# Kernel tuning notes

Measured on AMD Instinct MI355X. Metric: run time of the kernel, lower is better.

Reference implementation:

```python
import jax, jax.numpy as jnp
import numpy as np

BN_EPS = 1e-5


def setup_inputs() -> dict:
    key = jax.random.key(0)
    ks = jax.random.split(key, 8)
    N, C, T, V, M = 32, 64, 300, 25, 2
    O, S = 64, 3  # out_channels, num_subset
    x = jax.random.normal(ks[0], (N, C, T, V, M), jnp.float32)
    PA = jax.random.normal(ks[1], (S, V, V), jnp.float32) * 0.1
    conv_w = jax.random.normal(ks[2], (O * S, C), jnp.float32) * (1.0 / np.sqrt(C))
    conv_b = jax.random.normal(ks[3], (O * S,), jnp.float32) * 0.01
    bn_gamma = jnp.ones((O,), jnp.float32)
    bn_beta = jnp.zeros((O,), jnp.float32)
    bn_mean = jax.random.normal(ks[4], (O,), jnp.float32) * 0.1
    bn_var = jax.random.uniform(ks[5], (O,), jnp.float32, 0.5, 1.5)
    return {"x": x, "PA": PA, "conv_w": conv_w, "conv_b": conv_b,
            "bn_gamma": bn_gamma, "bn_beta": bn_beta,
            "bn_mean": bn_mean, "bn_var": bn_var}


def reference(x, PA, conv_w, conv_b, bn_gamma, bn_beta, bn_mean, bn_var):
    N, C, T, V, M = x.shape
    S = PA.shape[0]
    O = conv_w.shape[0] // S
    # (N, C, T, V, M) -> (N*M, C, T, V)
    xb = jnp.transpose(x, (0, 4, 1, 2, 3)).reshape(N * M, C, T, V)
    res = xb  # identity residual (in_channels == out_channels, stride == 1)
    # 1x1 conv == per-position matmul over channels
    y = jnp.einsum('bctv,oc->botv', xb, conv_w) + conv_b[None, :, None, None]
    y = y.reshape(N * M, S, O, T, V)
    # sum over subsets of per-subset adjacency mixes (fused einsum)
    z = jnp.einsum('bsctv,svw->bctw', y, PA)
    # BatchNorm2d (inference form with running stats)
    scale = bn_gamma / jnp.sqrt(bn_var + BN_EPS)
    z = z * scale[None, :, None, None] + (bn_beta - bn_mean * scale)[None, :, None, None]
    z = jax.nn.relu(z)
    out = jax.nn.relu(z + res)
    # (N*M, O, T, V) -> (N, O, T, V, M)
    return jnp.transpose(out.reshape(N, M, O, T, V), (0, 2, 3, 4, 1))
```

## Files before the change

### kernel.cpp

```cpp
#include <hip/hip_runtime.h>
#include <cstddef>
#include <cstdint>

#define N_  32
#define C_  64
#define T_  300
#define V_  25
#define M_  2
#define S_  3
#define O_  64
#define OS_ 192
#define TB  6
#define NT_BLK (T_/TB)
#define CTVM (C_*T_*V_*M_)
#define TVM  (T_*V_*M_)
#define VM   (V_*M_)
#define XPITCH 72
#define YPITCH 72

typedef short  short8  __attribute__((ext_vector_type(8)));
typedef float  float4_ __attribute__((ext_vector_type(4)));

__device__ __forceinline__ short f2bf(float f) {
    uint32_t u = __float_as_uint(f);
    u += 0x7FFFu + ((u >> 16) & 1u);
    return (short)(u >> 16);
}
__device__ __forceinline__ unsigned pk2bf(float a, float b) {
    const uint32_t ua = (uint32_t)(uint16_t)f2bf(a);
    const uint32_t ub = (uint32_t)(uint16_t)f2bf(b);
    return ua | (ub << 16);
}

__global__ void stgcn_prep(const float* __restrict__ Wc, const float* __restrict__ PA,
                           const float* __restrict__ g,  const float* __restrict__ b,
                           const float* __restrict__ mn, const float* __restrict__ vr,
                           short* __restrict__ Wb, short* __restrict__ PAb,
                           float* __restrict__ scl, float* __restrict__ sft)
{
    const int i = blockIdx.x * 256 + threadIdx.x;
    if (i < OS_ * C_) Wb[i] = f2bf(Wc[i]);
    const int r = i - OS_ * C_;
    if (r >= 0 && r < S_ * 32 * 32) {
        const int s = r >> 10, rem = r & 1023, wp = rem >> 5, vp = rem & 31;
        const float val = (wp < V_ && vp < V_) ? PA[s * V_ * V_ + vp * V_ + wp] : 0.0f;
        PAb[r] = f2bf(val);
    }
    const int q = r - S_ * 32 * 32;
    if (q >= 0 && q < O_) {
        const float sc = g[q] * rsqrtf(vr[q] + 1e-5f);
        scl[q] = sc;
        sft[q] = b[q] - mn[q] * sc;
    }
}

__global__ __launch_bounds__(256, 3)
void stgcn_main(const float* __restrict__ x, const float* __restrict__ cb,
                const short* __restrict__ Wb, const short* __restrict__ PAb,
                const float* __restrict__ sclg, const float* __restrict__ sftg,
                float* __restrict__ out)
{
    __shared__ short Xb[2][64 * XPITCH];
    __shared__ short Ys[OS_ * YPITCH];
    __shared__ float sclS[O_], sftS[O_];

    const int tid  = threadIdx.x;
    const int wv   = tid >> 6;
    const int lane = tid & 63;
    const int quad = lane >> 4;
    const int l15  = lane & 15;

    const int n  = blockIdx.x / NT_BLK;
    const int t0 = (blockIdx.x % NT_BLK) * TB;
    const size_t xbase = (size_t)n * CTVM;

    for (int i = tid; i < 2 * 14 * XPITCH; i += 256) {
        const int bf = i / (14 * XPITCH);
        const int r  = i - bf * (14 * XPITCH);
        const int pr = r / XPITCH, cc = r - pr * XPITCH;
        const int pos = (pr < 7) ? (25 + pr) : (50 + pr);
        Xb[bf][pos * XPITCH + cc] = 0;
    }
    if (tid < O_) { sclS[tid] = sclg[tid]; sftS[tid] = sftg[tid]; }

    const int wbase = wv * 48;
    short8 aW[3][2];
    #pragma unroll
    for (int mt = 0; mt < 3; ++mt)
        #pragma unroll
        for (int ks = 0; ks < 2; ++ks)
            aW[mt][ks] = *(const short8*)(Wb + (wbase + mt * 16 + l15) * C_ + ks * 32 + quad * 8);

    const int m2 = wv >> 1, hh = wv & 1;
    short8 bP[3];
    #pragma unroll
    for (int s = 0; s < 3; ++s)
        bP[s] = *(const short8*)(PAb + (s * 1024 + (hh * 16 + l15) * 32 + quad * 8));

    float cbw[3];
    #pragma unroll
    for (int mt = 0; mt < 3; ++mt) cbw[mt] = cb[wbase + mt * 16 + l15];

    {
        const float* xt = x + xbase + (size_t)t0 * VM;
        #pragma unroll
        for (int k = 0; k < 4; ++k) {
            const int p = tid + k * 256;
            if (p < 800) {
                const int v = p % 25, cp = p / 25;
                const float2 f0 = *(const float2*)(xt + (size_t)(2 * cp)     * TVM + v * 2);
                const float2 f1 = *(const float2*)(xt + (size_t)(2 * cp + 1) * TVM + v * 2);
                ((unsigned*)Xb[0])[v * 36 + cp]        = pk2bf(f0.x, f1.x);
                ((unsigned*)Xb[0])[(32 + v) * 36 + cp] = pk2bf(f0.y, f1.y);
            }
        }
    }

    int cur = 0;
    for (int tt = 0; tt < TB; ++tt) {
        __syncthreads();

        float2 R0[4], R1[4];
        const bool pf = (tt + 1 < TB);
        if (pf) {
            const float* xt = x + xbase + (size_t)(t0 + tt + 1) * VM;
            #pragma unroll
            for (int k = 0; k < 4; ++k) {
                const int p = tid + k * 256;
                if (p < 800) {
                    const int v = p % 25, cp = p / 25;
                    R0[k] = *(const float2*)(xt + (size_t)(2 * cp)     * TVM + v * 2);
                    R1[k] = *(const float2*)(xt + (size_t)(2 * cp + 1) * TVM + v * 2);
                }
            }
        }

        const short* Xc = Xb[cur];
        short8 bX[4][2];
        #pragma unroll
        for (int nt = 0; nt < 4; ++nt)
            #pragma unroll
            for (int ks = 0; ks < 2; ++ks)
                bX[nt][ks] = *(const short8*)(Xc + (nt * 16 + l15) * XPITCH + ks * 32 + quad * 8);

        #pragma unroll
        for (int mt = 0; mt < 3; ++mt) {
            #pragma unroll
            for (int nt = 0; nt < 4; ++nt) {
                float4_ acc = { cbw[mt], cbw[mt], cbw[mt], cbw[mt] };
                acc = __builtin_amdgcn_mfma_f32_16x16x32_bf16(bX[nt][0], aW[mt][0], acc, 0, 0, 0);
                acc = __builtin_amdgcn_mfma_f32_16x16x32_bf16(bX[nt][1], aW[mt][1], acc, 0, 0, 0);
                const int os = wbase + mt * 16 + l15;
                *(uint2*)(Ys + os * YPITCH + nt * 16 + quad * 4) =
                    make_uint2(pk2bf(acc[0], acc[1]), pk2bf(acc[2], acc[3]));
            }
        }
        __syncthreads();

        float4_ z[4];
        #pragma unroll
        for (int ot = 0; ot < 4; ++ot) { z[ot][0]=0.f; z[ot][1]=0.f; z[ot][2]=0.f; z[ot][3]=0.f; }
        #pragma unroll
        for (int s = 0; s < 3; ++s) {
            #pragma unroll
            for (int ot = 0; ot < 4; ++ot) {
                const short8 aY = *(const short8*)(Ys + (s * 64 + ot * 16 + l15) * YPITCH + m2 * 32 + quad * 8);
                z[ot] = __builtin_amdgcn_mfma_f32_16x16x32_bf16(aY, bP[s], z[ot], 0, 0, 0);
            }
        }

        const int wc = hh * 16 + l15;
        const int t  = t0 + tt;
        if (wc < V_) {
            const int xrow = (m2 * 32 + wc) * XPITCH;
            #pragma unroll
            for (int ot = 0; ot < 4; ++ot) {
                #pragma unroll
                for (int r = 0; r < 4; ++r) {
                    const int o = ot * 16 + quad * 4 + r;
                    const float res = __uint_as_float(((unsigned)(unsigned short)Xc[xrow + o]) << 16);
                    float q = fmaf(z[ot][r], sclS[o], sftS[o]);
                    q = fmaxf(q, 0.0f);
                    q = fmaxf(q + res, 0.0f);
                    out[xbase + (size_t)o * TVM + (size_t)t * VM + wc * 2 + m2] = q;
                }
            }
        }

        if (pf) {
            short* Xn = Xb[cur ^ 1];
            #pragma unroll
            for (int k = 0; k < 4; ++k) {
                const int p = tid + k * 256;
                if (p < 800) {
                    const int v = p % 25, cp = p / 25;
                    ((unsigned*)Xn)[v * 36 + cp]        = pk2bf(R0[k].x, R1[k].x);
                    ((unsigned*)Xn)[(32 + v) * 36 + cp] = pk2bf(R0[k].y, R1[k].y);
                }
            }
        }
        cur ^= 1;
    }
}

extern "C" void kernel_launch(void* const* d_in, const int* in_sizes, int n_in,
                              void* d_out, int out_size, void* d_ws, size_t ws_size,
                              hipStream_t stream)
{
    const float* x    = (const float*)d_in[0];
    const float* PA   = (const float*)d_in[1];
    const float* Wc   = (const float*)d_in[2];
    const float* cb   = (const float*)d_in[3];
    const float* bn_g = (const float*)d_in[4];
    const float* bn_b = (const float*)d_in[5];
    const float* bn_m = (const float*)d_in[6];
    const float* bn_v = (const float*)d_in[7];
    float* out = (float*)d_out;

    char* ws = (char*)d_ws;
    short* Wb  = (short*)ws;
    short* PAb = (short*)(ws + 24576);
    float* scl = (float*)(ws + 30720);
    float* sft = (float*)(ws + 30976);

    stgcn_prep<<<61, 256, 0, stream>>>(Wc, PA, bn_g, bn_b, bn_m, bn_v, Wb, PAb, scl, sft);
    stgcn_main<<<N_ * NT_BLK, 256, 0, stream>>>(x, cb, Wb, PAb, scl, sft, out);
}
```

Measured before the change: 289.5 us.

## Fuse prep into main kernel, use per-wave Y staging, deepen x prefetch

Drops the separate prep launch: each block now converts the weights, adjacency matrix and BN parameters to bf16/scale form directly from fp32 inputs. The work is repartitioned so each wave computes all three subsets for its own 16 output channels and stages Y in a private LDS slice. This removes the mid-iteration block-wide barrier, leaving only one barrier per time step. Global x prefetch goes two timesteps ahead, and stores are paired across M into float2 writes. In exchange, every block repeats the parameter conversion and holds more registers for the prefetch buffers, which may pressure occupancy.

```diff
diff --git a/kernel.cpp b/kernel.cpp
--- a/kernel.cpp
+++ b/kernel.cpp
@@ -9,7 +9,6 @@
 #define M_  2
 #define S_  3
 #define O_  64
-#define OS_ 192
 #define TB  6
 #define NT_BLK (T_/TB)
 #define CTVM (C_*T_*V_*M_)
@@ -27,41 +26,24 @@
     return (short)(u >> 16);
 }
 __device__ __forceinline__ unsigned pk2bf(float a, float b) {
-    const uint32_t ua = (uint32_t)(uint16_t)f2bf(a);
-    const uint32_t ub = (uint32_t)(uint16_t)f2bf(b);
-    return ua | (ub << 16);
-}
-
-__global__ void stgcn_prep(const float* __restrict__ Wc, const float* __restrict__ PA,
-                           const float* __restrict__ g,  const float* __restrict__ b,
-                           const float* __restrict__ mn, const float* __restrict__ vr,
-                           short* __restrict__ Wb, short* __restrict__ PAb,
-                           float* __restrict__ scl, float* __restrict__ sft)
-{
-    const int i = blockIdx.x * 256 + threadIdx.x;
-    if (i < OS_ * C_) Wb[i] = f2bf(Wc[i]);
-    const int r = i - OS_ * C_;
-    if (r >= 0 && r < S_ * 32 * 32) {
-        const int s = r >> 10, rem = r & 1023, wp = rem >> 5, vp = rem & 31;
-        const float val = (wp < V_ && vp < V_) ? PA[s * V_ * V_ + vp * V_ + wp] : 0.0f;
-        PAb[r] = f2bf(val);
-    }
-    const int q = r - S_ * 32 * 32;
-    if (q >= 0 && q < O_) {
-        const float sc = g[q] * rsqrtf(vr[q] + 1e-5f);
-        scl[q] = sc;
-        sft[q] = b[q] - mn[q] * sc;
-    }
+    return (uint32_t)(uint16_t)f2bf(a) | ((uint32_t)(uint16_t)f2bf(b) << 16);
+}
+__device__ __forceinline__ void barrier_lgkm() {
+    asm volatile("s_waitcnt lgkmcnt(0)\n\ts_barrier" ::: "memory");
+}
+__device__ __forceinline__ void wait_lgkm() {
+    asm volatile("s_waitcnt lgkmcnt(0)" ::: "memory");
 }
 
 __global__ __launch_bounds__(256, 3)
-void stgcn_main(const float* __restrict__ x, const float* __restrict__ cb,
-                const short* __restrict__ Wb, const short* __restrict__ PAb,
-                const float* __restrict__ sclg, const float* __restrict__ sftg,
-                float* __restrict__ out)
+void stgcn_fused(const float* __restrict__ x,  const float* __restrict__ PA,
+                 const float* __restrict__ Wc, const float* __restrict__ cb,
+                 const float* __restrict__ g,  const float* __restrict__ bb,
+                 const float* __restrict__ mn, const float* __restrict__ vr,
+                 float* __restrict__ out)
 {
     __shared__ short Xb[2][64 * XPITCH];
-    __shared__ short Ys[OS_ * YPITCH];
+    __shared__ short Ysw[4 * 48 * YPITCH];
     __shared__ float sclS[O_], sftS[O_];
 
     const int tid  = threadIdx.x;
@@ -69,10 +51,70 @@
     const int lane = tid & 63;
     const int quad = lane >> 4;
     const int l15  = lane & 15;
+    const int ybase = wv * 48 * YPITCH;
 
     const int n  = blockIdx.x / NT_BLK;
     const int t0 = (blockIdx.x % NT_BLK) * TB;
     const size_t xbase = (size_t)n * CTVM;
+
+    float2 P0[4], P1[4];
+    float2 Rx[2][4], Ry[2][4];
+    {
+        const float* xt = x + xbase + (size_t)t0 * VM;
+        #pragma unroll
+        for (int k = 0; k < 4; ++k) {
+            const int p = tid + k * 256;
+            if (p < 800) {
+                const int v = p % 25, cp = p / 25;
+                P0[k] = *(const float2*)(xt + (size_t)(2 * cp)     * TVM + v * 2);
+                P1[k] = *(const float2*)(xt + (size_t)(2 * cp + 1) * TVM + v * 2);
+                Rx[0][k] = *(const float2*)(xt + (size_t)(2 * cp)     * TVM + VM + v * 2);
+                Ry[0][k] = *(const float2*)(xt + (size_t)(2 * cp + 1) * TVM + VM + v * 2);
+            }
+        }
+    }
+
+    short8 aW[3][2];
+    #pragma unroll
+    for (int s = 0; s < 3; ++s)
+        #pragma unroll
+        for (int ks = 0; ks < 2; ++ks) {
+            const float* wr = Wc + (size_t)(s * 64 + wv * 16 + l15) * C_ + ks * 32 + quad * 8;
+            const float4 wa = *(const float4*)wr;
+            const float4 wb = *(const float4*)(wr + 4);
+            union { short8 s8; unsigned u[4]; } r;
+            r.u[0] = pk2bf(wa.x, wa.y); r.u[1] = pk2bf(wa.z, wa.w);
+            r.u[2] = pk2bf(wb.x, wb.y); r.u[3] = pk2bf(wb.z, wb.w);
+            aW[s][ks] = r.s8;
+        }
+
+    short8 bP[3][2];
+    #pragma unroll
+    for (int s = 0; s < 3; ++s)
+        #pragma unroll
+        for (int wt = 0; wt < 2; ++wt) {
+            const int w = wt * 16 + l15;
+            float pv[8];
+            #pragma unroll
+            for (int j = 0; j < 8; ++j) {
+                const int v = quad * 8 + j;
+                pv[j] = (w < V_ && v < V_) ? PA[s * V_ * V_ + v * V_ + w] : 0.0f;
+            }
+            union { short8 s8; unsigned u[4]; } r;
+            r.u[0] = pk2bf(pv[0], pv[1]); r.u[1] = pk2bf(pv[2], pv[3]);
+            r.u[2] = pk2bf(pv[4], pv[5]); r.u[3] = pk2bf(pv[6], pv[7]);
+            bP[s][wt] = r.s8;
+        }
+
+    float cbw[3];
+    #pragma unroll
+    for (int s = 0; s < 3; ++s) cbw[s] = cb[s * 64 + wv * 16 + l15];
+
+    if (tid < O_) {
+        const float sc = g[tid] * rsqrtf(vr[tid] + 1e-5f);
+        sclS[tid] = sc;
+        sftS[tid] = bb[tid] - mn[tid] * sc;
+    }
 
     for (int i = tid; i < 2 * 14 * XPITCH; i += 256) {
         const int bf = i / (14 * XPITCH);
@@ -81,56 +123,37 @@
         const int pos = (pr < 7) ? (25 + pr) : (50 + pr);
         Xb[bf][pos * XPITCH + cc] = 0;
     }
-    if (tid < O_) { sclS[tid] = sclg[tid]; sftS[tid] = sftg[tid]; }
-
-    const int wbase = wv * 48;
-    short8 aW[3][2];
-    #pragma unroll
-    for (int mt = 0; mt < 3; ++mt)
-        #pragma unroll
-        for (int ks = 0; ks < 2; ++ks)
-            aW[mt][ks] = *(const short8*)(Wb + (wbase + mt * 16 + l15) * C_ + ks * 32 + quad * 8);
-
-    const int m2 = wv >> 1, hh = wv & 1;
-    short8 bP[3];
-    #pragma unroll
-    for (int s = 0; s < 3; ++s)
-        bP[s] = *(const short8*)(PAb + (s * 1024 + (hh * 16 + l15) * 32 + quad * 8));
-
-    float cbw[3];
-    #pragma unroll
-    for (int mt = 0; mt < 3; ++mt) cbw[mt] = cb[wbase + mt * 16 + l15];
-
-    {
-        const float* xt = x + xbase + (size_t)t0 * VM;
-        #pragma unroll
-        for (int k = 0; k < 4; ++k) {
-            const int p = tid + k * 256;
-            if (p < 800) {
-                const int v = p % 25, cp = p / 25;
-                const float2 f0 = *(const float2*)(xt + (size_t)(2 * cp)     * TVM + v * 2);
-                const float2 f1 = *(const float2*)(xt + (size_t)(2 * cp + 1) * TVM + v * 2);
-                ((unsigned*)Xb[0])[v * 36 + cp]        = pk2bf(f0.x, f1.x);
-                ((unsigned*)Xb[0])[(32 + v) * 36 + cp] = pk2bf(f0.y, f1.y);
-            }
-        }
-    }
-
-    int cur = 0;
-    for (int tt = 0; tt < TB; ++tt) {
-        __syncthreads();
-
-        float2 R0[4], R1[4];
-        const bool pf = (tt + 1 < TB);
-        if (pf) {
-            const float* xt = x + xbase + (size_t)(t0 + tt + 1) * VM;
+
+    #pragma unroll
+    for (int k = 0; k < 4; ++k) {
+        const int p = tid + k * 256;
+        if (p < 800) {
+            const int v = p % 25, cp = p / 25;
+            ((unsigned*)Xb[0])[v * 36 + cp]        = pk2bf(P0[k].x, P1[k].x);
+            ((unsigned*)Xb[0])[(32 + v) * 36 + cp] = pk2bf(P0[k].y, P1[k].y);
+        }
+    }
+    barrier_lgkm();
+
+    const float4 sclr = *(const float4*)&sclS[wv * 16 + quad * 4];
+    const float4 sftr = *(const float4*)&sftS[wv * 16 + quad * 4];
+    const float sclA[4] = { sclr.x, sclr.y, sclr.z, sclr.w };
+    const float sftA[4] = { sftr.x, sftr.y, sftr.z, sftr.w };
+
+    for (int i = 0; i < TB; ++i) {
+        const int t   = t0 + i;
+        const int cur = i & 1, nxt = cur ^ 1;
+
+        if (i + 2 < TB) {
+            const float* xt = x + xbase + (size_t)(t + 2) * VM;
+            const int sl = (i + 1) & 1;
             #pragma unroll
             for (int k = 0; k < 4; ++k) {
                 const int p = tid + k * 256;
                 if (p < 800) {
                     const int v = p % 25, cp = p / 25;
-                    R0[k] = *(const float2*)(xt + (size_t)(2 * cp)     * TVM + v * 2);
-                    R1[k] = *(const float2*)(xt + (size_t)(2 * cp + 1) * TVM + v * 2);
+                    Rx[sl][k] = *(const float2*)(xt + (size_t)(2 * cp)     * TVM + v * 2);
+                    Ry[sl][k] = *(const float2*)(xt + (size_t)(2 * cp + 1) * TVM + v * 2);
                 }
             }
         }
@@ -144,62 +167,66 @@
                 bX[nt][ks] = *(const short8*)(Xc + (nt * 16 + l15) * XPITCH + ks * 32 + quad * 8);
 
         #pragma unroll
-        for (int mt = 0; mt < 3; ++mt) {
+        for (int s = 0; s < 3; ++s) {
             #pragma unroll
             for (int nt = 0; nt < 4; ++nt) {
-                float4_ acc = { cbw[mt], cbw[mt], cbw[mt], cbw[mt] };
-                acc = __builtin_amdgcn_mfma_f32_16x16x32_bf16(bX[nt][0], aW[mt][0], acc, 0, 0, 0);
-                acc = __builtin_amdgcn_mfma_f32_16x16x32_bf16(bX[nt][1], aW[mt][1], acc, 0, 0, 0);
-                const int os = wbase + mt * 16 + l15;
-                *(uint2*)(Ys + os * YPITCH + nt * 16 + quad * 4) =
+                float4_ acc = { cbw[s], cbw[s], cbw[s], cbw[s] };
+                acc = __builtin_amdgcn_mfma_f32_16x16x32_bf16(bX[nt][0], aW[s][0], acc, 0, 0, 0);
+                acc = __builtin_amdgcn_mfma_f32_16x16x32_bf16(bX[nt][1], aW[s][1], acc, 0, 0, 0);
+                *(uint2*)(Ysw + ybase + (s * 16 + l15) * YPITCH + nt * 16 + quad * 4) =
                     make_uint2(pk2bf(acc[0], acc[1]), pk2bf(acc[2], acc[3]));
             }
         }
-        __syncthreads();
-
-        float4_ z[4];
-        #pragma unroll
-        for (int ot = 0; ot < 4; ++ot) { z[ot][0]=0.f; z[ot][1]=0.f; z[ot][2]=0.f; z[ot][3]=0.f; }
-        #pragma unroll
-        for (int s = 0; s < 3; ++s) {
-            #pragma unroll
-            for (int ot = 0; ot < 4; ++ot) {
-                const short8 aY = *(const short8*)(Ys + (s * 64 + ot * 16 + l15) * YPITCH + m2 * 32 + quad * 8);
-                z[ot] = __builtin_amdgcn_mfma_f32_16x16x32_bf16(aY, bP[s], z[ot], 0, 0, 0);
-            }
-        }
-
-        const int wc = hh * 16 + l15;
-        const int t  = t0 + tt;
-        if (wc < V_) {
-            const int xrow = (m2 * 32 + wc) * XPITCH;
-            #pragma unroll
-            for (int ot = 0; ot < 4; ++ot) {
+        wait_lgkm();
+
+        float4_ z[2][2];
+        #pragma unroll
+        for (int m = 0; m < 2; ++m)
+            #pragma unroll
+            for (int wt = 0; wt < 2; ++wt)
+                { z[m][wt][0]=0.f; z[m][wt][1]=0.f; z[m][wt][2]=0.f; z[m][wt][3]=0.f; }
+        #pragma unroll
+        for (int m = 0; m < 2; ++m) {
+            #pragma unroll
+            for (int s = 0; s < 3; ++s) {
+                const short8 aY = *(const short8*)(Ysw + ybase + (s * 16 + l15) * YPITCH + m * 32 + quad * 8);
+                z[m][0] = __builtin_amdgcn_mfma_f32_16x16x32_bf16(aY, bP[s][0], z[m][0], 0, 0, 0);
+                z[m][1] = __builtin_amdgcn_mfma_f32_16x16x32_bf16(aY, bP[s][1], z[m][1], 0, 0, 0);
+            }
+        }
+
+        #pragma unroll
+        for (int wt = 0; wt < 2; ++wt) {
+            const int wc = wt * 16 + l15;
+            if (wc < V_) {
                 #pragma unroll
                 for (int r = 0; r < 4; ++r) {
-                    const int o = ot * 16 + quad * 4 + r;
-                    const float res = __uint_as_float(((unsigned)(unsigned short)Xc[xrow + o]) << 16);
-                    float q = fmaf(z[ot][r], sclS[o], sftS[o]);
-                    q = fmaxf(q, 0.0f);
-                    q = fmaxf(q + res, 0.0f);
-                    out[xbase + (size_t)o * TVM + (size_t)t * VM + wc * 2 + m2] = q;
+                    const int o = wv * 16 + quad * 4 + r;
+                    const float r0 = __uint_as_float(((unsigned)(unsigned short)Xc[(wc)      * XPITCH + o]) << 16);
+                    const float r1 = __uint_as_float(((unsigned)(unsigned short)Xc[(32 + wc) * XPITCH + o]) << 16);
+                    float q0 = fmaf(z[0][wt][r], sclA[r], sftA[r]);
+                    float q1 = fmaf(z[1][wt][r], sclA[r], sftA[r]);
+                    q0 = fmaxf(fmaxf(q0, 0.0f) + r0, 0.0f);
+                    q1 = fmaxf(fmaxf(q1, 0.0f) + r1, 0.0f);
+                    *(float2*)(out + xbase + (size_t)o * TVM + (size_t)t * VM + wc * 2) =
+                        make_float2(q0, q1);
                 }
             }
         }
 
-        if (pf) {
-            short* Xn = Xb[cur ^ 1];
+        if (i + 1 < TB) {
+            const int sl = i & 1;
             #pragma unroll
             for (int k = 0; k < 4; ++k) {
                 const int p = tid + k * 256;
                 if (p < 800) {
                     const int v = p % 25, cp = p / 25;
-                    ((unsigned*)Xn)[v * 36 + cp]        = pk2bf(R0[k].x, R1[k].x);
-                    ((unsigned*)Xn)[(32 + v) * 36 + cp] = pk2bf(R0[k].y, R1[k].y);
+                    ((unsigned*)Xb[nxt])[v * 36 + cp]        = pk2bf(Rx[sl][k].x, Ry[sl][k].x);
+                    ((unsigned*)Xb[nxt])[(32 + v) * 36 + cp] = pk2bf(Rx[sl][k].y, Ry[sl][k].y);
                 }
             }
         }
-        cur ^= 1;
+        barrier_lgkm();
     }
 }
 
@@ -217,12 +244,5 @@
     const float* bn_v = (const float*)d_in[7];
     float* out = (float*)d_out;
 
-    char* ws = (char*)d_ws;
-    short* Wb  = (short*)ws;
-    short* PAb = (short*)(ws + 24576);
-    float* scl = (float*)(ws + 30720);
-    float* sft = (float*)(ws + 30976);
-
-    stgcn_prep<<<61, 256, 0, stream>>>(Wc, PA, bn_g, bn_b, bn_m, bn_v, Wb, PAb, scl, sft);
-    stgcn_main<<<N_ * NT_BLK, 256, 0, stream>>>(x, cb, Wb, PAb, scl, sft, out);
-}
+    stgcn_fused<<<N_ * NT_BLK, 256, 0, stream>>>(x, PA, Wc, cb, bn_g, bn_b, bn_m, bn_v, out);
+}
```

Result: slower. 339.0 us (+17.1%).

## Give each wave its own output-channel slice and pair M outputs in stores

Applied to the files above, without the earlier changes.

Work is re-split so each wave owns 16 output channels across all three subsets and both M slices. The intermediate Y buffer becomes wave-private, and the graph-mix result for both M values is produced per lane, so stores write float2 pairs instead of stride-2 scalars. The X buffer drops from double to single buffering, BN scale/shift move from shared memory into registers, and launch bounds rise to 4 blocks per SM. The aim is less LDS use, higher occupancy and better-coalesced global writes. The cost is more register pressure and the loss of overlap that double buffering gave.

```diff
diff --git a/kernel.cpp b/kernel.cpp
--- a/kernel.cpp
+++ b/kernel.cpp
@@ -27,9 +27,13 @@
     return (short)(u >> 16);
 }
 __device__ __forceinline__ unsigned pk2bf(float a, float b) {
-    const uint32_t ua = (uint32_t)(uint16_t)f2bf(a);
-    const uint32_t ub = (uint32_t)(uint16_t)f2bf(b);
-    return ua | (ub << 16);
+    return (uint32_t)(uint16_t)f2bf(a) | ((uint32_t)(uint16_t)f2bf(b) << 16);
+}
+__device__ __forceinline__ void barrier_lgkm() {
+    asm volatile("s_waitcnt lgkmcnt(0)\n\ts_barrier" ::: "memory");
+}
+__device__ __forceinline__ float bf2f(unsigned bits16) {
+    return __uint_as_float(bits16 << 16);
 }
 
 __global__ void stgcn_prep(const float* __restrict__ Wc, const float* __restrict__ PA,
@@ -54,52 +58,54 @@
     }
 }
 
-__global__ __launch_bounds__(256, 3)
+__global__ __launch_bounds__(256, 4)
 void stgcn_main(const float* __restrict__ x, const float* __restrict__ cb,
                 const short* __restrict__ Wb, const short* __restrict__ PAb,
                 const float* __restrict__ sclg, const float* __restrict__ sftg,
                 float* __restrict__ out)
 {
-    __shared__ short Xb[2][64 * XPITCH];
-    __shared__ short Ys[OS_ * YPITCH];
-    __shared__ float sclS[O_], sftS[O_];
+    __shared__ short Xb[64 * XPITCH];
+    __shared__ short Ysw[4 * 48 * YPITCH];
 
     const int tid  = threadIdx.x;
     const int wv   = tid >> 6;
     const int lane = tid & 63;
     const int quad = lane >> 4;
     const int l15  = lane & 15;
+    const int ybase = wv * 48 * YPITCH;
 
     const int n  = blockIdx.x / NT_BLK;
     const int t0 = (blockIdx.x % NT_BLK) * TB;
     const size_t xbase = (size_t)n * CTVM;
 
-    for (int i = tid; i < 2 * 14 * XPITCH; i += 256) {
-        const int bf = i / (14 * XPITCH);
-        const int r  = i - bf * (14 * XPITCH);
-        const int pr = r / XPITCH, cc = r - pr * XPITCH;
-        const int pos = (pr < 7) ? (25 + pr) : (50 + pr);
-        Xb[bf][pos * XPITCH + cc] = 0;
-    }
-    if (tid < O_) { sclS[tid] = sclg[tid]; sftS[tid] = sftg[tid]; }
-
-    const int wbase = wv * 48;
     short8 aW[3][2];
     #pragma unroll
-    for (int mt = 0; mt < 3; ++mt)
+    for (int s = 0; s < 3; ++s)
         #pragma unroll
         for (int ks = 0; ks < 2; ++ks)
-            aW[mt][ks] = *(const short8*)(Wb + (wbase + mt * 16 + l15) * C_ + ks * 32 + quad * 8);
-
-    const int m2 = wv >> 1, hh = wv & 1;
-    short8 bP[3];
+            aW[s][ks] = *(const short8*)(Wb + (s * 64 + wv * 16 + l15) * C_ + ks * 32 + quad * 8);
+
+    short8 bP[3][2];
     #pragma unroll
     for (int s = 0; s < 3; ++s)
-        bP[s] = *(const short8*)(PAb + (s * 1024 + (hh * 16 + l15) * 32 + quad * 8));
+        #pragma unroll
+        for (int wt = 0; wt < 2; ++wt)
+            bP[s][wt] = *(const short8*)(PAb + s * 1024 + (wt * 16 + l15) * 32 + quad * 8);
 
     float cbw[3];
     #pragma unroll
-    for (int mt = 0; mt < 3; ++mt) cbw[mt] = cb[wbase + mt * 16 + l15];
+    for (int s = 0; s < 3; ++s) cbw[s] = cb[s * 64 + wv * 16 + l15];
+
+    const float4 sclr = *(const float4*)&sclg[wv * 16 + quad * 4];
+    const float4 sftr = *(const float4*)&sftg[wv * 16 + quad * 4];
+    const float sclA[4] = { sclr.x, sclr.y, sclr.z, sclr.w };
+    const float sftA[4] = { sftr.x, sftr.y, sftr.z, sftr.w };
+
+    for (int i = tid; i < 14 * XPITCH; i += 256) {
+        const int pr = i / XPITCH, cc = i - pr * XPITCH;
+        const int pos = (pr < 7) ? (25 + pr) : (50 + pr);
+        Xb[pos * XPITCH + cc] = 0;
+    }
 
     {
         const float* xt = x + xbase + (size_t)t0 * VM;
@@ -110,96 +116,103 @@
                 const int v = p % 25, cp = p / 25;
                 const float2 f0 = *(const float2*)(xt + (size_t)(2 * cp)     * TVM + v * 2);
                 const float2 f1 = *(const float2*)(xt + (size_t)(2 * cp + 1) * TVM + v * 2);
-                ((unsigned*)Xb[0])[v * 36 + cp]        = pk2bf(f0.x, f1.x);
-                ((unsigned*)Xb[0])[(32 + v) * 36 + cp] = pk2bf(f0.y, f1.y);
-            }
-        }
-    }
-
-    int cur = 0;
-    for (int tt = 0; tt < TB; ++tt) {
-        __syncthreads();
-
-        float2 R0[4], R1[4];
-        const bool pf = (tt + 1 < TB);
+                ((unsigned*)Xb)[v * 36 + cp]        = pk2bf(f0.x, f1.x);
+                ((unsigned*)Xb)[(32 + v) * 36 + cp] = pk2bf(f0.y, f1.y);
+            }
+        }
+    }
+
+    for (int i = 0; i < TB; ++i) {
+        const int t = t0 + i;
+        barrier_lgkm();
+
+        float2 Rx[4], Ry[4];
+        const bool pf = (i + 1 < TB);
         if (pf) {
-            const float* xt = x + xbase + (size_t)(t0 + tt + 1) * VM;
+            const float* xt = x + xbase + (size_t)(t + 1) * VM;
             #pragma unroll
             for (int k = 0; k < 4; ++k) {
                 const int p = tid + k * 256;
                 if (p < 800) {
                     const int v = p % 25, cp = p / 25;
-                    R0[k] = *(const float2*)(xt + (size_t)(2 * cp)     * TVM + v * 2);
-                    R1[k] = *(const float2*)(xt + (size_t)(2 * cp + 1) * TVM + v * 2);
+                    Rx[k] = *(const float2*)(xt + (size_t)(2 * cp)     * TVM + v * 2);
+                    Ry[k] = *(const float2*)(xt + (size_t)(2 * cp + 1) * TVM + v * 2);
                 }
             }
         }
 
-        const short* Xc = Xb[cur];
-        short8 bX[4][2];
-        #pragma unroll
-        for (int nt = 0; nt < 4; ++nt)
-            #pragma unroll
-            for (int ks = 0; ks < 2; ++ks)
-                bX[nt][ks] = *(const short8*)(Xc + (nt * 16 + l15) * XPITCH + ks * 32 + quad * 8);
-
-        #pragma unroll
-        for (int mt = 0; mt < 3; ++mt) {
-            #pragma unroll
-            for (int nt = 0; nt < 4; ++nt) {
-                float4_ acc = { cbw[mt], cbw[mt], cbw[mt], cbw[mt] };
-                acc = __builtin_amdgcn_mfma_f32_16x16x32_bf16(bX[nt][0], aW[mt][0], acc, 0, 0, 0);
-                acc = __builtin_amdgcn_mfma_f32_16x16x32_bf16(bX[nt][1], aW[mt][1], acc, 0, 0, 0);
-                const int os = wbase + mt * 16 + l15;
-                *(uint2*)(Ys + os * YPITCH + nt * 16 + quad * 4) =
+        uint2 resp[2][2];
+        #pragma unroll
+        for (int m = 0; m < 2; ++m)
+            #pragma unroll
+            for (int wt = 0; wt < 2; ++wt)
+                resp[m][wt] = *(const uint2*)(Xb + (m * 32 + wt * 16 + l15) * XPITCH
+                                                 + wv * 16 + quad * 4);
+
+        #pragma unroll
+        for (int nt = 0; nt < 4; ++nt) {
+            const short8 b0 = *(const short8*)(Xb + (nt * 16 + l15) * XPITCH + quad * 8);
+            const short8 b1 = *(const short8*)(Xb + (nt * 16 + l15) * XPITCH + 32 + quad * 8);
+            #pragma unroll
+            for (int s = 0; s < 3; ++s) {
+                float4_ acc = { cbw[s], cbw[s], cbw[s], cbw[s] };
+                acc = __builtin_amdgcn_mfma_f32_16x16x32_bf16(b0, aW[s][0], acc, 0, 0, 0);
+                acc = __builtin_amdgcn_mfma_f32_16x16x32_bf16(b1, aW[s][1], acc, 0, 0, 0);
+                *(uint2*)(Ysw + ybase + (s * 16 + l15) * YPITCH + nt * 16 + quad * 4) =
                     make_uint2(pk2bf(acc[0], acc[1]), pk2bf(acc[2], acc[3]));
             }
         }
-        __syncthreads();
-
-        float4_ z[4];
-        #pragma unroll
-        for (int ot = 0; ot < 4; ++ot) { z[ot][0]=0.f; z[ot][1]=0.f; z[ot][2]=0.f; z[ot][3]=0.f; }
-        #pragma unroll
-        for (int s = 0; s < 3; ++s) {
-            #pragma unroll
-            for (int ot = 0; ot < 4; ++ot) {
-                const short8 aY = *(const short8*)(Ys + (s * 64 + ot * 16 + l15) * YPITCH + m2 * 32 + quad * 8);
-                z[ot] = __builtin_amdgcn_mfma_f32_16x16x32_bf16(aY, bP[s], z[ot], 0, 0, 0);
-            }
-        }
-
-        const int wc = hh * 16 + l15;
-        const int t  = t0 + tt;
-        if (wc < V_) {
-            const int xrow = (m2 * 32 + wc) * XPITCH;
-            #pragma unroll
-            for (int ot = 0; ot < 4; ++ot) {
+        barrier_lgkm();
+
+        float4_ z[2][2];
+        #pragma unroll
+        for (int m = 0; m < 2; ++m)
+            #pragma unroll
+            for (int wt = 0; wt < 2; ++wt)
+                { z[m][wt][0]=0.f; z[m][wt][1]=0.f; z[m][wt][2]=0.f; z[m][wt][3]=0.f; }
+        #pragma unroll
+        for (int m = 0; m < 2; ++m) {
+            #pragma unroll
+            for (int s = 0; s < 3; ++s) {
+                const short8 aY = *(const short8*)(Ysw + ybase + (s * 16 + l15) * YPITCH
+                                                       + m * 32 + quad * 8);
+                z[m][0] = __builtin_amdgcn_mfma_f32_16x16x32_bf16(aY, bP[s][0], z[m][0], 0, 0, 0);
+                z[m][1] = __builtin_amdgcn_mfma_f32_16x16x32_bf16(aY, bP[s][1], z[m][1], 0, 0, 0);
+            }
+        }
+
+        #pragma unroll
+        for (int wt = 0; wt < 2; ++wt) {
+            const int wc = wt * 16 + l15;
+            if (wc < V_) {
                 #pragma unroll
                 for (int r = 0; r < 4; ++r) {
-                    const int o = ot * 16 + quad * 4 + r;
-                    const float res = __uint_as_float(((unsigned)(unsigned short)Xc[xrow + o]) << 16);
-                    float q = fmaf(z[ot][r], sclS[o], sftS[o]);
-                    q = fmaxf(q, 0.0f);
-                    q = fmaxf(q + res, 0.0f);
-                    out[xbase + (size_t)o * TVM + (size_t)t * VM + wc * 2 + m2] = q;
+                    const int o = wv * 16 + quad * 4 + r;
+                    const unsigned pr0 = (r < 2) ? resp[0][wt].x : resp[0][wt].y;
+                    const unsigned pr1 = (r < 2) ? resp[1][wt].x : resp[1][wt].y;
+                    const float r0 = bf2f((r & 1) ? (pr0 >> 16) : (pr0 & 0xFFFFu));
+                    const float r1 = bf2f((r & 1) ? (pr1 >> 16) : (pr1 & 0xFFFFu));
+                    float q0 = fmaf(z[0][wt][r], sclA[r], sftA[r]);
+                    float q1 = fmaf(z[1][wt][r], sclA[r], sftA[r]);
+                    q0 = fmaxf(fmaxf(q0, 0.0f) + r0, 0.0f);
+                    q1 = fmaxf(fmaxf(q1, 0.0f) + r1, 0.0f);
+                    *(float2*)(out + xbase + (size_t)o * TVM + (size_t)t * VM + wc * 2) =
+                        make_float2(q0, q1);
                 }
             }
         }
 
         if (pf) {
-            short* Xn = Xb[cur ^ 1];
             #pragma unroll
             for (int k = 0; k < 4; ++k) {
                 const int p = tid + k * 256;
                 if (p < 800) {
                     const int v = p % 25, cp = p / 25;
-                    ((unsigned*)Xn)[v * 36 + cp]        = pk2bf(R0[k].x, R1[k].x);
-                    ((unsigned*)Xn)[(32 + v) * 36 + cp] = pk2bf(R0[k].y, R1[k].y);
+                    ((unsigned*)Xb)[v * 36 + cp]        = pk2bf(Rx[k].x, Ry[k].x);
+                    ((unsigned*)Xb)[(32 + v) * 36 + cp] = pk2bf(Rx[k].y, Ry[k].y);
                 }
             }
         }
-        cur ^= 1;
     }
 }
 
```

Result: slower. 324.7 us (+12.2%).
